# Kernel tuning notes

Measured on AMD Instinct MI355X. Metric: run time of the kernel, lower is better.

Reference implementation:

```python
import jax, jax.numpy as jnp
import numpy as np

B, S, D, A = 16, 4096, 2048, 2048

def setup_inputs() -> dict:
    key = jax.random.key(0)
    k1, k2, k3, k4 = jax.random.split(key, 4)
    encode_state = jax.random.normal(k1, (B, S, D), dtype=jnp.float32)
    hid_state = jax.random.normal(k2, (B, D), dtype=jnp.float32)
    W = jax.random.normal(k3, (A, D), dtype=jnp.float32) * (1.0 / np.sqrt(D))
    b = jax.random.normal(k4, (A,), dtype=jnp.float32) * 0.01
    return {"encode_state": encode_state, "hid_state": hid_state, "W": W, "b": b}

def reference(encode_state, hid_state, W, b):
    # project both encoder states and decoder hidden state: y = x @ W.T + b
    enc_proj = jnp.einsum('bsd,ad->bsa', encode_state, W) + b   # [B,S,A]
    hid_proj = jnp.einsum('bd,ad->ba', hid_state, W) + b        # [B,A]
    scores = jnp.einsum('bsa,ba->bs', enc_proj, hid_proj)       # [B,S]
    probs = jax.nn.softmax(scores, axis=1)                      # softmax over seq dim
    context_vector = jnp.einsum('bs,bsd->bd', probs, encode_state)  # [B,D]
    return (scores, context_vector)
```

## Files before the change

### kernel.cpp

```cpp
#include <hip/hip_runtime.h>
#include <cstddef>

#define BB 16
#define SS 4096
#define DD 2048
#define AA 2048
#define CH 128
#define ACH 64

__global__ __launch_bounds__(256) void hp_kernel(
    const float* __restrict__ hid, const float* __restrict__ W,
    const float* __restrict__ bias, float* __restrict__ hp) {
  int gw   = (blockIdx.x * 256 + threadIdx.x) >> 6;
  int lane = threadIdx.x & 63;
  int a = gw;
  const float4* Wr = reinterpret_cast<const float4*>(W + (size_t)a * DD);
  float acc[BB];
#pragma unroll
  for (int b = 0; b < BB; ++b) acc[b] = 0.f;
#pragma unroll
  for (int k = 0; k < 8; ++k) {
    float4 w4 = Wr[lane + 64 * k];
#pragma unroll
    for (int b = 0; b < BB; ++b) {
      float4 h4 = reinterpret_cast<const float4*>(hid + b * DD)[lane + 64 * k];
      acc[b] += w4.x * h4.x + w4.y * h4.y + w4.z * h4.z + w4.w * h4.w;
    }
  }
  float bi = bias[a];
#pragma unroll
  for (int b = 0; b < BB; ++b) {
    float s = acc[b];
#pragma unroll
    for (int off = 32; off; off >>= 1) s += __shfl_xor(s, off, 64);
    if (lane == 0) hp[b * AA + a] = s + bi;
  }
}

__global__ __launch_bounds__(256) void vpart_kernel(
    const float* __restrict__ hp, const float* __restrict__ W,
    float* __restrict__ vpart) {
  int t  = threadIdx.x;
  int ac = blockIdx.x & 63;
  int dc = blockIdx.x >> 6;
  int d0 = dc * 1024 + 4 * t;
  float4 acc[BB];
#pragma unroll
  for (int b = 0; b < BB; ++b) acc[b] = make_float4(0.f, 0.f, 0.f, 0.f);
  int abase = ac * 32;
  for (int i = 0; i < 32; ++i) {
    int a = abase + i;
    float4 w4 = *reinterpret_cast<const float4*>(W + (size_t)a * DD + d0);
#pragma unroll
    for (int b = 0; b < BB; ++b) {
      float h = hp[b * AA + a];
      acc[b].x += h * w4.x; acc[b].y += h * w4.y;
      acc[b].z += h * w4.z; acc[b].w += h * w4.w;
    }
  }
#pragma unroll
  for (int b = 0; b < BB; ++b)
    *reinterpret_cast<float4*>(vpart + (size_t)(ac * BB + b) * DD + d0) = acc[b];
}

__global__ __launch_bounds__(256) void c_kernel(
    const float* __restrict__ hp, const float* __restrict__ bias,
    float* __restrict__ cvec) {
  int b = blockIdx.x, t = threadIdx.x;
  float s = 0.f;
  for (int i = t; i < AA; i += 256) s += bias[i] * hp[b * AA + i];
#pragma unroll
  for (int off = 32; off; off >>= 1) s += __shfl_xor(s, off, 64);
  __shared__ float red[4];
  if ((t & 63) == 0) red[t >> 6] = s;
  __syncthreads();
  if (t == 0) cvec[b] = red[0] + red[1] + red[2] + red[3];
}

__global__ __launch_bounds__(256) void reducev_kernel(
    const float* __restrict__ vpart, float* __restrict__ v) {
  int i = blockIdx.x * 256 + threadIdx.x;
  float s = 0.f;
#pragma unroll
  for (int c = 0; c < ACH; ++c) s += vpart[(size_t)c * (BB * DD) + i];
  v[i] = s;
}

__global__ __launch_bounds__(256) void fused_kernel(
    const float* __restrict__ enc, const float* __restrict__ v,
    const float* __restrict__ cvec, float* __restrict__ scores,
    float* __restrict__ mpart, float* __restrict__ lpart,
    float* __restrict__ ctxpart) {
  int gw   = blockIdx.x * 4 + (threadIdx.x >> 6);
  int lane = threadIdx.x & 63;
  int b  = gw >> 7;
  int ch = gw & (CH - 1);
  const float4* vp = reinterpret_cast<const float4*>(v + b * DD);
  float4 vf[8];
#pragma unroll
  for (int k = 0; k < 8; ++k) vf[k] = vp[lane + 64 * k];
  float cb = cvec[b];
  float4 acc[8];
#pragma unroll
  for (int k = 0; k < 8; ++k) acc[k] = make_float4(0.f, 0.f, 0.f, 0.f);
  float m = -1e30f, l = 0.f, myscore = 0.f;
  size_t rowbase = (size_t)(b * SS + ch * 32) * DD;
  for (int r = 0; r < 32; ++r) {
    const float4* ep = reinterpret_cast<const float4*>(enc + rowbase + (size_t)r * DD);
    float4 e[8];
#pragma unroll
    for (int k = 0; k < 8; ++k) e[k] = ep[lane + 64 * k];
    float dot = 0.f;
#pragma unroll
    for (int k = 0; k < 8; ++k)
      dot += e[k].x * vf[k].x + e[k].y * vf[k].y + e[k].z * vf[k].z + e[k].w * vf[k].w;
#pragma unroll
    for (int off = 32; off; off >>= 1) dot += __shfl_xor(dot, off, 64);
    float score = dot + cb;
    if (lane == r) myscore = score;
    float mnew  = fmaxf(m, score);
    float scale = __expf(m - mnew);
    float p     = __expf(score - mnew);
    l = l * scale + p;
#pragma unroll
    for (int k = 0; k < 8; ++k) {
      acc[k].x = acc[k].x * scale + p * e[k].x;
      acc[k].y = acc[k].y * scale + p * e[k].y;
      acc[k].z = acc[k].z * scale + p * e[k].z;
      acc[k].w = acc[k].w * scale + p * e[k].w;
    }
    m = mnew;
  }
  if (lane < 32) scores[b * SS + ch * 32 + lane] = myscore;
  if (lane == 0) { mpart[gw] = m; lpart[gw] = l; }
  float4* cp = reinterpret_cast<float4*>(ctxpart + (size_t)gw * DD);
#pragma unroll
  for (int k = 0; k < 8; ++k) cp[lane + 64 * k] = acc[k];
}

__global__ __launch_bounds__(128) void mstats_kernel(
    const float* __restrict__ mpart, const float* __restrict__ lpart,
    float* __restrict__ wnorm) {
  int b = blockIdx.x, t = threadIdx.x;
  float mt = mpart[b * CH + t];
  float lt = lpart[b * CH + t];
  float M = mt;
#pragma unroll
  for (int off = 32; off; off >>= 1) M = fmaxf(M, __shfl_xor(M, off, 64));
  __shared__ float sm[2];
  if ((t & 63) == 0) sm[t >> 6] = M;
  __syncthreads();
  M = fmaxf(sm[0], sm[1]);
  float w  = __expf(mt - M);
  float lw = lt * w;
#pragma unroll
  for (int off = 32; off; off >>= 1) lw += __shfl_xor(lw, off, 64);
  __shared__ float sl[2];
  if ((t & 63) == 0) sl[t >> 6] = lw;
  __syncthreads();
  float L = sl[0] + sl[1];
  wnorm[b * CH + t] = w / L;
}

__global__ __launch_bounds__(256) void combine1_kernel(
    const float* __restrict__ ctxpart, const float* __restrict__ wnorm,
    float* __restrict__ part2) {
  int b = blockIdx.x >> 3;
  int g = blockIdx.x & 7;
  int t = threadIdx.x;
  float4 a0 = make_float4(0.f, 0.f, 0.f, 0.f);
  float4 a1 = make_float4(0.f, 0.f, 0.f, 0.f);
  for (int i = 0; i < 16; ++i) {
    int c = g * 16 + i;
    float w = wnorm[b * CH + c];
    const float4* cp = reinterpret_cast<const float4*>(ctxpart + (size_t)(b * CH + c) * DD);
    float4 e0 = cp[t];
    float4 e1 = cp[t + 256];
    a0.x += w * e0.x; a0.y += w * e0.y; a0.z += w * e0.z; a0.w += w * e0.w;
    a1.x += w * e1.x; a1.y += w * e1.y; a1.z += w * e1.z; a1.w += w * e1.w;
  }
  float4* o = reinterpret_cast<float4*>(part2 + (size_t)(b * 8 + g) * DD);
  o[t] = a0;
  o[t + 256] = a1;
}

__global__ __launch_bounds__(256) void combine2_kernel(
    const float* __restrict__ part2, float* __restrict__ ctx) {
  int i = blockIdx.x * 256 + threadIdx.x;
  int b = i >> 11;
  int d = i & 2047;
  float s = 0.f;
#pragma unroll
  for (int g = 0; g < 8; ++g) s += part2[(size_t)(b * 8 + g) * DD + d];
  ctx[i] = s;
}

extern "C" void kernel_launch(void* const* d_in, const int* in_sizes, int n_in,
                              void* d_out, int out_size, void* d_ws, size_t ws_size,
                              hipStream_t stream) {
  const float* enc  = (const float*)d_in[0];
  const float* hid  = (const float*)d_in[1];
  const float* W    = (const float*)d_in[2];
  const float* bias = (const float*)d_in[3];

  float* out_scores = (float*)d_out;
  float* out_ctx    = (float*)d_out + BB * SS;

  float* ws    = (float*)d_ws;
  float* hp    = ws;
  float* vpart = hp + BB * AA;
  float* v     = vpart + ACH * BB * DD;
  float* cvec  = v + BB * DD;
  float* mpart = cvec + BB;
  float* lpart = mpart + BB * CH;
  float* wnorm = lpart + BB * CH;
  float* ctxp  = wnorm + BB * CH;
  float* part2 = ctxp + (size_t)BB * CH * DD;

  hipLaunchKernelGGL(hp_kernel,      dim3(512), dim3(256), 0, stream, hid, W, bias, hp);
  hipLaunchKernelGGL(vpart_kernel,   dim3(128), dim3(256), 0, stream, hp, W, vpart);
  hipLaunchKernelGGL(c_kernel,       dim3(16),  dim3(256), 0, stream, hp, bias, cvec);
  hipLaunchKernelGGL(reducev_kernel, dim3(128), dim3(256), 0, stream, vpart, v);
  hipLaunchKernelGGL(fused_kernel,   dim3(512), dim3(256), 0, stream,
                     enc, v, cvec, out_scores, mpart, lpart, ctxp);
  hipLaunchKernelGGL(mstats_kernel,  dim3(16),  dim3(128), 0, stream, mpart, lpart, wnorm);
  hipLaunchKernelGGL(combine1_kernel, dim3(128), dim3(256), 0, stream, ctxp, wnorm, part2);
  hipLaunchKernelGGL(combine2_kernel, dim3(128), dim3(256), 0, stream, part2, out_ctx);
}
```

Before: 205.3 us.

## Double-buffer encoder rows, halve rows per wave, store partial contexts as bf16

The fused attention kernel now handles 16 rows per wave instead of 32, doubling the grid, and prefetches the next encoder row into a second register buffer while it computes on the current one. The v vector is reloaded from memory on each step instead of being kept in registers, and launch bounds ask for 4 blocks per CU to raise occupancy. Per-wave partial contexts are written as packed bf16, halving that intermediate traffic, and the combine and stats kernels are adjusted for 256 chunks. The cost is bf16 rounding in the context partials, plus twice as much partial data to reduce.

```diff
diff --git a/kernel.cpp b/kernel.cpp
--- a/kernel.cpp
+++ b/kernel.cpp
@@ -1,12 +1,19 @@
 #include <hip/hip_runtime.h>
+#include <hip/hip_bf16.h>
 #include <cstddef>
 
 #define BB 16
 #define SS 4096
 #define DD 2048
 #define AA 2048
-#define CH 128
+#define NR 16
+#define CH 256
 #define ACH 64
+
+__device__ inline unsigned int pk_bf16(float a, float b) {
+  __hip_bfloat162 h2 = __float22bfloat162_rn(make_float2(a, b));
+  return *reinterpret_cast<unsigned int*>(&h2);
+}
 
 __global__ __launch_bounds__(256) void hp_kernel(
     const float* __restrict__ hid, const float* __restrict__ W,
@@ -86,59 +93,78 @@
   v[i] = s;
 }
 
-__global__ __launch_bounds__(256) void fused_kernel(
+__global__ __launch_bounds__(256, 4) void fused_kernel(
     const float* __restrict__ enc, const float* __restrict__ v,
     const float* __restrict__ cvec, float* __restrict__ scores,
     float* __restrict__ mpart, float* __restrict__ lpart,
-    float* __restrict__ ctxpart) {
+    unsigned int* __restrict__ ctxpart ) {
   int gw   = blockIdx.x * 4 + (threadIdx.x >> 6);
   int lane = threadIdx.x & 63;
-  int b  = gw >> 7;
+  int b  = gw >> 8;
   int ch = gw & (CH - 1);
   const float4* vp = reinterpret_cast<const float4*>(v + b * DD);
-  float4 vf[8];
-#pragma unroll
-  for (int k = 0; k < 8; ++k) vf[k] = vp[lane + 64 * k];
   float cb = cvec[b];
   float4 acc[8];
 #pragma unroll
   for (int k = 0; k < 8; ++k) acc[k] = make_float4(0.f, 0.f, 0.f, 0.f);
   float m = -1e30f, l = 0.f, myscore = 0.f;
-  size_t rowbase = (size_t)(b * SS + ch * 32) * DD;
-  for (int r = 0; r < 32; ++r) {
-    const float4* ep = reinterpret_cast<const float4*>(enc + rowbase + (size_t)r * DD);
-    float4 e[8];
-#pragma unroll
-    for (int k = 0; k < 8; ++k) e[k] = ep[lane + 64 * k];
-    float dot = 0.f;
-#pragma unroll
-    for (int k = 0; k < 8; ++k)
-      dot += e[k].x * vf[k].x + e[k].y * vf[k].y + e[k].z * vf[k].z + e[k].w * vf[k].w;
-#pragma unroll
-    for (int off = 32; off; off >>= 1) dot += __shfl_xor(dot, off, 64);
-    float score = dot + cb;
-    if (lane == r) myscore = score;
-    float mnew  = fmaxf(m, score);
-    float scale = __expf(m - mnew);
-    float p     = __expf(score - mnew);
-    l = l * scale + p;
-#pragma unroll
-    for (int k = 0; k < 8; ++k) {
-      acc[k].x = acc[k].x * scale + p * e[k].x;
-      acc[k].y = acc[k].y * scale + p * e[k].y;
-      acc[k].z = acc[k].z * scale + p * e[k].z;
-      acc[k].w = acc[k].w * scale + p * e[k].w;
-    }
-    m = mnew;
-  }
-  if (lane < 32) scores[b * SS + ch * 32 + lane] = myscore;
+  const float4* rowp = reinterpret_cast<const float4*>(
+      enc + (size_t)(b * SS + ch * NR) * DD);
+  float4 eA[8], eB[8];
+#pragma unroll
+  for (int k = 0; k < 8; ++k) eA[k] = rowp[lane + 64 * k];
+
+#define STEP(CUR, NXT, R)                                                     \
+  {                                                                           \
+    int rn = ((R) + 1 < NR) ? (R) + 1 : (R);                                  \
+    _Pragma("unroll")                                                         \
+    for (int k = 0; k < 8; ++k)                                               \
+      NXT[k] = rowp[(size_t)rn * 512 + lane + 64 * k];                        \
+    float dot = 0.f;                                                          \
+    _Pragma("unroll")                                                         \
+    for (int k = 0; k < 8; ++k) {                                             \
+      float4 vv = vp[lane + 64 * k];                                          \
+      dot += CUR[k].x * vv.x + CUR[k].y * vv.y + CUR[k].z * vv.z +            \
+             CUR[k].w * vv.w;                                                 \
+    }                                                                         \
+    _Pragma("unroll")                                                         \
+    for (int off = 32; off; off >>= 1) dot += __shfl_xor(dot, off, 64);       \
+    float score = dot + cb;                                                   \
+    if (lane == (R)) myscore = score;                                         \
+    float mnew  = fmaxf(m, score);                                            \
+    float scale = __expf(m - mnew);                                           \
+    float p     = __expf(score - mnew);                                       \
+    l = l * scale + p;                                                        \
+    _Pragma("unroll")                                                         \
+    for (int k = 0; k < 8; ++k) {                                             \
+      acc[k].x = acc[k].x * scale + p * CUR[k].x;                             \
+      acc[k].y = acc[k].y * scale + p * CUR[k].y;                             \
+      acc[k].z = acc[k].z * scale + p * CUR[k].z;                             \
+      acc[k].w = acc[k].w * scale + p * CUR[k].w;                             \
+    }                                                                         \
+    m = mnew;                                                                 \
+  }
+
+#pragma unroll
+  for (int rr = 0; rr < NR; rr += 2) {
+    STEP(eA, eB, rr)
+    STEP(eB, eA, rr + 1)
+  }
+#undef STEP
+
+  if (lane < NR) scores[b * SS + ch * NR + lane] = myscore;
   if (lane == 0) { mpart[gw] = m; lpart[gw] = l; }
-  float4* cp = reinterpret_cast<float4*>(ctxpart + (size_t)gw * DD);
-#pragma unroll
-  for (int k = 0; k < 8; ++k) cp[lane + 64 * k] = acc[k];
-}
-
-__global__ __launch_bounds__(128) void mstats_kernel(
+  uint2* cp = reinterpret_cast<uint2*>(ctxpart) + (size_t)gw * 512;
+#pragma unroll
+  for (int k = 0; k < 8; ++k) {
+    uint2 u;
+    u.x = pk_bf16(acc[k].x, acc[k].y);
+    u.y = pk_bf16(acc[k].z, acc[k].w);
+    cp[lane + 64 * k] = u;
+  }
+}
+
+__global__ __launch_bounds__(256) void mstats_kernel(
     const float* __restrict__ mpart, const float* __restrict__ lpart,
     float* __restrict__ wnorm) {
   int b = blockIdx.x, t = threadIdx.x;
@@ -147,41 +173,47 @@
   float M = mt;
 #pragma unroll
   for (int off = 32; off; off >>= 1) M = fmaxf(M, __shfl_xor(M, off, 64));
-  __shared__ float sm[2];
+  __shared__ float sm[4];
   if ((t & 63) == 0) sm[t >> 6] = M;
   __syncthreads();
-  M = fmaxf(sm[0], sm[1]);
+  M = fmaxf(fmaxf(sm[0], sm[1]), fmaxf(sm[2], sm[3]));
   float w  = __expf(mt - M);
   float lw = lt * w;
 #pragma unroll
   for (int off = 32; off; off >>= 1) lw += __shfl_xor(lw, off, 64);
-  __shared__ float sl[2];
+  __shared__ float sl[4];
   if ((t & 63) == 0) sl[t >> 6] = lw;
   __syncthreads();
-  float L = sl[0] + sl[1];
+  float L = sl[0] + sl[1] + sl[2] + sl[3];
   wnorm[b * CH + t] = w / L;
 }
 
 __global__ __launch_bounds__(256) void combine1_kernel(
-    const float* __restrict__ ctxpart, const float* __restrict__ wnorm,
+    const unsigned int* __restrict__ ctxpart, const float* __restrict__ wnorm,
     float* __restrict__ part2) {
-  int b = blockIdx.x >> 3;
-  int g = blockIdx.x & 7;
+  int b = blockIdx.x >> 4;
+  int g = blockIdx.x & 15;
   int t = threadIdx.x;
-  float4 a0 = make_float4(0.f, 0.f, 0.f, 0.f);
-  float4 a1 = make_float4(0.f, 0.f, 0.f, 0.f);
+  float a0 = 0.f, a1 = 0.f, a2 = 0.f, a3 = 0.f;
+  float a4 = 0.f, a5 = 0.f, a6 = 0.f, a7 = 0.f;
   for (int i = 0; i < 16; ++i) {
     int c = g * 16 + i;
     float w = wnorm[b * CH + c];
-    const float4* cp = reinterpret_cast<const float4*>(ctxpart + (size_t)(b * CH + c) * DD);
-    float4 e0 = cp[t];
-    float4 e1 = cp[t + 256];
-    a0.x += w * e0.x; a0.y += w * e0.y; a0.z += w * e0.z; a0.w += w * e0.w;
-    a1.x += w * e1.x; a1.y += w * e1.y; a1.z += w * e1.z; a1.w += w * e1.w;
-  }
-  float4* o = reinterpret_cast<float4*>(part2 + (size_t)(b * 8 + g) * DD);
-  o[t] = a0;
-  o[t + 256] = a1;
+    const uint4* p = reinterpret_cast<const uint4*>(
+        ctxpart + (size_t)(b * CH + c) * (DD / 2));
+    uint4 q = p[t];
+    a0 += w * __uint_as_float(q.x << 16);
+    a1 += w * __uint_as_float(q.x & 0xffff0000u);
+    a2 += w * __uint_as_float(q.y << 16);
+    a3 += w * __uint_as_float(q.y & 0xffff0000u);
+    a4 += w * __uint_as_float(q.z << 16);
+    a5 += w * __uint_as_float(q.z & 0xffff0000u);
+    a6 += w * __uint_as_float(q.w << 16);
+    a7 += w * __uint_as_float(q.w & 0xffff0000u);
+  }
+  float4* o = reinterpret_cast<float4*>(part2 + (size_t)(b * 16 + g) * DD + 8 * t);
+  o[0] = make_float4(a0, a1, a2, a3);
+  o[1] = make_float4(a4, a5, a6, a7);
 }
 
 __global__ __launch_bounds__(256) void combine2_kernel(
@@ -191,7 +223,7 @@
   int d = i & 2047;
   float s = 0.f;
 #pragma unroll
-  for (int g = 0; g < 8; ++g) s += part2[(size_t)(b * 8 + g) * DD + d];
+  for (int g = 0; g < 16; ++g) s += part2[(size_t)(b * 16 + g) * DD + d];
   ctx[i] = s;
 }
 
@@ -214,16 +246,16 @@
   float* mpart = cvec + BB;
   float* lpart = mpart + BB * CH;
   float* wnorm = lpart + BB * CH;
-  float* ctxp  = wnorm + BB * CH;
-  float* part2 = ctxp + (size_t)BB * CH * DD;
-
-  hipLaunchKernelGGL(hp_kernel,      dim3(512), dim3(256), 0, stream, hid, W, bias, hp);
-  hipLaunchKernelGGL(vpart_kernel,   dim3(128), dim3(256), 0, stream, hp, W, vpart);
-  hipLaunchKernelGGL(c_kernel,       dim3(16),  dim3(256), 0, stream, hp, bias, cvec);
-  hipLaunchKernelGGL(reducev_kernel, dim3(128), dim3(256), 0, stream, vpart, v);
-  hipLaunchKernelGGL(fused_kernel,   dim3(512), dim3(256), 0, stream,
+  unsigned int* ctxp = (unsigned int*)(wnorm + BB * CH);
+  float* part2 = (float*)(ctxp + (size_t)BB * CH * DD / 2);
+
+  hipLaunchKernelGGL(hp_kernel,      dim3(512),  dim3(256), 0, stream, hid, W, bias, hp);
+  hipLaunchKernelGGL(vpart_kernel,   dim3(128),  dim3(256), 0, stream, hp, W, vpart);
+  hipLaunchKernelGGL(c_kernel,       dim3(16),   dim3(256), 0, stream, hp, bias, cvec);
+  hipLaunchKernelGGL(reducev_kernel, dim3(128),  dim3(256), 0, stream, vpart, v);
+  hipLaunchKernelGGL(fused_kernel,   dim3(1024), dim3(256), 0, stream,
                      enc, v, cvec, out_scores, mpart, lpart, ctxp);
-  hipLaunchKernelGGL(mstats_kernel,  dim3(16),  dim3(128), 0, stream, mpart, lpart, wnorm);
-  hipLaunchKernelGGL(combine1_kernel, dim3(128), dim3(256), 0, stream, ctxp, wnorm, part2);
+  hipLaunchKernelGGL(mstats_kernel,  dim3(16),   dim3(256), 0, stream, mpart, lpart, wnorm);
+  hipLaunchKernelGGL(combine1_kernel, dim3(256), dim3(256), 0, stream, ctxp, wnorm, part2);
   hipLaunchKernelGGL(combine2_kernel, dim3(128), dim3(256), 0, stream, part2, out_ctx);
 }
```

Measured after the change: 449.7 us. +119.0%, slower.

## Halve rows per wave, lazily rescale softmax, store bf16 partials, merge small kernels

Applied to the files above, without the earlier changes.

The fused streaming kernel now handles 16 rows per wave with double the waves, for more parallelism over the encoder read. Online softmax now rescales the accumulator only when the score exceeds the running max by more than 40, which drops most per-row exp and multiply work. Context partials are stored as packed bf16 to halve the partial write and read traffic. The small kernels are merged: c and reducev become one finalize launch, and mstats plus the two combine passes become one epilogue, cutting launches from eight to five. The cost is bf16 rounding in the partial context sums and more partial rows to reduce.

```diff
diff --git a/kernel.cpp b/kernel.cpp
--- a/kernel.cpp
+++ b/kernel.cpp
@@ -1,12 +1,19 @@
 #include <hip/hip_runtime.h>
+#include <hip/hip_bf16.h>
 #include <cstddef>
 
 #define BB 16
 #define SS 4096
 #define DD 2048
 #define AA 2048
-#define CH 128
+#define NR 16
+#define CH 256
 #define ACH 64
+
+__device__ inline unsigned int pk_bf16(float a, float b) {
+  __hip_bfloat162 h2 = __float22bfloat162_rn(make_float2(a, b));
+  return *reinterpret_cast<unsigned int*>(&h2);
+}
 
 __global__ __launch_bounds__(256) void hp_kernel(
     const float* __restrict__ hid, const float* __restrict__ W,
@@ -63,136 +70,131 @@
     *reinterpret_cast<float4*>(vpart + (size_t)(ac * BB + b) * DD + d0) = acc[b];
 }
 
-__global__ __launch_bounds__(256) void c_kernel(
-    const float* __restrict__ hp, const float* __restrict__ bias,
+__global__ __launch_bounds__(256) void finalize_kernel(
+    const float* __restrict__ vpart, const float* __restrict__ hp,
+    const float* __restrict__ bias, float* __restrict__ v,
     float* __restrict__ cvec) {
-  int b = blockIdx.x, t = threadIdx.x;
-  float s = 0.f;
-  for (int i = t; i < AA; i += 256) s += bias[i] * hp[b * AA + i];
-#pragma unroll
-  for (int off = 32; off; off >>= 1) s += __shfl_xor(s, off, 64);
-  __shared__ float red[4];
-  if ((t & 63) == 0) red[t >> 6] = s;
-  __syncthreads();
-  if (t == 0) cvec[b] = red[0] + red[1] + red[2] + red[3];
-}
-
-__global__ __launch_bounds__(256) void reducev_kernel(
-    const float* __restrict__ vpart, float* __restrict__ v) {
-  int i = blockIdx.x * 256 + threadIdx.x;
-  float s = 0.f;
-#pragma unroll
-  for (int c = 0; c < ACH; ++c) s += vpart[(size_t)c * (BB * DD) + i];
-  v[i] = s;
+  if (blockIdx.x < 128) {
+    int i = blockIdx.x * 256 + threadIdx.x;
+    float s = 0.f;
+#pragma unroll
+    for (int c = 0; c < ACH; ++c) s += vpart[(size_t)c * (BB * DD) + i];
+    v[i] = s;
+  } else {
+    int b = blockIdx.x - 128;
+    int t = threadIdx.x;
+    float s = 0.f;
+    for (int i = t; i < AA; i += 256) s += bias[i] * hp[b * AA + i];
+#pragma unroll
+    for (int off = 32; off; off >>= 1) s += __shfl_xor(s, off, 64);
+    __shared__ float red[4];
+    if ((t & 63) == 0) red[t >> 6] = s;
+    __syncthreads();
+    if (t == 0) cvec[b] = red[0] + red[1] + red[2] + red[3];
+  }
 }
 
 __global__ __launch_bounds__(256) void fused_kernel(
     const float* __restrict__ enc, const float* __restrict__ v,
     const float* __restrict__ cvec, float* __restrict__ scores,
     float* __restrict__ mpart, float* __restrict__ lpart,
-    float* __restrict__ ctxpart) {
+    unsigned int* __restrict__ ctxpart ) {
   int gw   = blockIdx.x * 4 + (threadIdx.x >> 6);
   int lane = threadIdx.x & 63;
-  int b  = gw >> 7;
+  int b  = gw >> 8;
   int ch = gw & (CH - 1);
-  const float4* vp = reinterpret_cast<const float4*>(v + b * DD);
-  float4 vf[8];
-#pragma unroll
-  for (int k = 0; k < 8; ++k) vf[k] = vp[lane + 64 * k];
+  const float4* vp = reinterpret_cast<const float4*>(v + (size_t)b * DD);
   float cb = cvec[b];
   float4 acc[8];
 #pragma unroll
   for (int k = 0; k < 8; ++k) acc[k] = make_float4(0.f, 0.f, 0.f, 0.f);
-  float m = -1e30f, l = 0.f, myscore = 0.f;
-  size_t rowbase = (size_t)(b * SS + ch * 32) * DD;
-  for (int r = 0; r < 32; ++r) {
-    const float4* ep = reinterpret_cast<const float4*>(enc + rowbase + (size_t)r * DD);
+  float m_s = -1e30f;
+  float l = 0.f, myscore = 0.f;
+  const float4* rowp = reinterpret_cast<const float4*>(
+      enc + (size_t)(b * SS + ch * NR) * DD);
+
+#pragma unroll
+  for (int r = 0; r < NR; ++r) {
     float4 e[8];
 #pragma unroll
-    for (int k = 0; k < 8; ++k) e[k] = ep[lane + 64 * k];
+    for (int k = 0; k < 8; ++k) e[k] = rowp[(size_t)r * 512 + lane + 64 * k];
     float dot = 0.f;
 #pragma unroll
-    for (int k = 0; k < 8; ++k)
-      dot += e[k].x * vf[k].x + e[k].y * vf[k].y + e[k].z * vf[k].z + e[k].w * vf[k].w;
+    for (int k = 0; k < 8; ++k) {
+      float4 vv = vp[lane + 64 * k];
+      dot += e[k].x * vv.x + e[k].y * vv.y + e[k].z * vv.z + e[k].w * vv.w;
+    }
 #pragma unroll
     for (int off = 32; off; off >>= 1) dot += __shfl_xor(dot, off, 64);
     float score = dot + cb;
     if (lane == r) myscore = score;
-    float mnew  = fmaxf(m, score);
-    float scale = __expf(m - mnew);
-    float p     = __expf(score - mnew);
-    l = l * scale + p;
+    if (score > m_s + 40.f) {
+      float rs = __expf(m_s - score);
+      l *= rs;
+#pragma unroll
+      for (int k = 0; k < 8; ++k) {
+        acc[k].x *= rs; acc[k].y *= rs; acc[k].z *= rs; acc[k].w *= rs;
+      }
+      m_s = score;
+    }
+    float p = __expf(score - m_s);
+    l += p;
 #pragma unroll
     for (int k = 0; k < 8; ++k) {
-      acc[k].x = acc[k].x * scale + p * e[k].x;
-      acc[k].y = acc[k].y * scale + p * e[k].y;
-      acc[k].z = acc[k].z * scale + p * e[k].z;
-      acc[k].w = acc[k].w * scale + p * e[k].w;
-    }
-    m = mnew;
-  }
-  if (lane < 32) scores[b * SS + ch * 32 + lane] = myscore;
-  if (lane == 0) { mpart[gw] = m; lpart[gw] = l; }
-  float4* cp = reinterpret_cast<float4*>(ctxpart + (size_t)gw * DD);
-#pragma unroll
-  for (int k = 0; k < 8; ++k) cp[lane + 64 * k] = acc[k];
-}
-
-__global__ __launch_bounds__(128) void mstats_kernel(
+      acc[k].x += p * e[k].x;
+      acc[k].y += p * e[k].y;
+      acc[k].z += p * e[k].z;
+      acc[k].w += p * e[k].w;
+    }
+  }
+
+  if (lane < NR) scores[b * SS + ch * NR + lane] = myscore;
+  if (lane == 0) { mpart[gw] = m_s; lpart[gw] = l; }
+  uint2* cp = reinterpret_cast<uint2*>(ctxpart) + (size_t)gw * 512;
+#pragma unroll
+  for (int k = 0; k < 8; ++k) {
+    uint2 u;
+    u.x = pk_bf16(acc[k].x, acc[k].y);
+    u.y = pk_bf16(acc[k].z, acc[k].w);
+    cp[lane + 64 * k] = u;
+  }
+}
+
+__global__ __launch_bounds__(256) void epilogue_kernel(
     const float* __restrict__ mpart, const float* __restrict__ lpart,
-    float* __restrict__ wnorm) {
-  int b = blockIdx.x, t = threadIdx.x;
+    const unsigned int* __restrict__ ctxpart, float* __restrict__ ctx) {
+  int b  = blockIdx.x >> 3;
+  int ds = blockIdx.x & 7;
+  int t  = threadIdx.x;
+  __shared__ float wsm[CH];
+  __shared__ float redm[4], redl[4];
   float mt = mpart[b * CH + t];
   float lt = lpart[b * CH + t];
   float M = mt;
 #pragma unroll
   for (int off = 32; off; off >>= 1) M = fmaxf(M, __shfl_xor(M, off, 64));
-  __shared__ float sm[2];
-  if ((t & 63) == 0) sm[t >> 6] = M;
+  if ((t & 63) == 0) redm[t >> 6] = M;
   __syncthreads();
-  M = fmaxf(sm[0], sm[1]);
+  M = fmaxf(fmaxf(redm[0], redm[1]), fmaxf(redm[2], redm[3]));
   float w  = __expf(mt - M);
   float lw = lt * w;
 #pragma unroll
   for (int off = 32; off; off >>= 1) lw += __shfl_xor(lw, off, 64);
-  __shared__ float sl[2];
-  if ((t & 63) == 0) sl[t >> 6] = lw;
+  if ((t & 63) == 0) redl[t >> 6] = lw;
   __syncthreads();
-  float L = sl[0] + sl[1];
-  wnorm[b * CH + t] = w / L;
-}
-
-__global__ __launch_bounds__(256) void combine1_kernel(
-    const float* __restrict__ ctxpart, const float* __restrict__ wnorm,
-    float* __restrict__ part2) {
-  int b = blockIdx.x >> 3;
-  int g = blockIdx.x & 7;
-  int t = threadIdx.x;
-  float4 a0 = make_float4(0.f, 0.f, 0.f, 0.f);
-  float4 a1 = make_float4(0.f, 0.f, 0.f, 0.f);
-  for (int i = 0; i < 16; ++i) {
-    int c = g * 16 + i;
-    float w = wnorm[b * CH + c];
-    const float4* cp = reinterpret_cast<const float4*>(ctxpart + (size_t)(b * CH + c) * DD);
-    float4 e0 = cp[t];
-    float4 e1 = cp[t + 256];
-    a0.x += w * e0.x; a0.y += w * e0.y; a0.z += w * e0.z; a0.w += w * e0.w;
-    a1.x += w * e1.x; a1.y += w * e1.y; a1.z += w * e1.z; a1.w += w * e1.w;
-  }
-  float4* o = reinterpret_cast<float4*>(part2 + (size_t)(b * 8 + g) * DD);
-  o[t] = a0;
-  o[t + 256] = a1;
-}
-
-__global__ __launch_bounds__(256) void combine2_kernel(
-    const float* __restrict__ part2, float* __restrict__ ctx) {
-  int i = blockIdx.x * 256 + threadIdx.x;
-  int b = i >> 11;
-  int d = i & 2047;
-  float s = 0.f;
-#pragma unroll
-  for (int g = 0; g < 8; ++g) s += part2[(size_t)(b * 8 + g) * DD + d];
-  ctx[i] = s;
+  float L = redl[0] + redl[1] + redl[2] + redl[3];
+  wsm[t] = w / L;
+  __syncthreads();
+  int du = ds * 128 + (t >> 1);
+  bool hi = (t & 1);
+  float acc = 0.f;
+  const unsigned int* base = ctxpart + (size_t)(b * CH) * (DD / 2) + du;
+  for (int c = 0; c < CH; ++c) {
+    unsigned int u = base[(size_t)c * (DD / 2)];
+    float e = __uint_as_float(hi ? (u & 0xffff0000u) : (u << 16));
+    acc += wsm[c] * e;
+  }
+  ctx[b * DD + ds * 256 + t] = acc;
 }
 
 extern "C" void kernel_launch(void* const* d_in, const int* in_sizes, int n_in,
@@ -213,17 +215,13 @@
   float* cvec  = v + BB * DD;
   float* mpart = cvec + BB;
   float* lpart = mpart + BB * CH;
-  float* wnorm = lpart + BB * CH;
-  float* ctxp  = wnorm + BB * CH;
-  float* part2 = ctxp + (size_t)BB * CH * DD;
-
-  hipLaunchKernelGGL(hp_kernel,      dim3(512), dim3(256), 0, stream, hid, W, bias, hp);
-  hipLaunchKernelGGL(vpart_kernel,   dim3(128), dim3(256), 0, stream, hp, W, vpart);
-  hipLaunchKernelGGL(c_kernel,       dim3(16),  dim3(256), 0, stream, hp, bias, cvec);
-  hipLaunchKernelGGL(reducev_kernel, dim3(128), dim3(256), 0, stream, vpart, v);
-  hipLaunchKernelGGL(fused_kernel,   dim3(512), dim3(256), 0, stream,
+  unsigned int* ctxp = (unsigned int*)(lpart + BB * CH);
+
+  hipLaunchKernelGGL(hp_kernel,       dim3(512),  dim3(256), 0, stream, hid, W, bias, hp);
+  hipLaunchKernelGGL(vpart_kernel,    dim3(128),  dim3(256), 0, stream, hp, W, vpart);
+  hipLaunchKernelGGL(finalize_kernel, dim3(144),  dim3(256), 0, stream, vpart, hp, bias, v, cvec);
+  hipLaunchKernelGGL(fused_kernel,    dim3(1024), dim3(256), 0, stream,
                      enc, v, cvec, out_scores, mpart, lpart, ctxp);
-  hipLaunchKernelGGL(mstats_kernel,  dim3(16),  dim3(128), 0, stream, mpart, lpart, wnorm);
-  hipLaunchKernelGGL(combine1_kernel, dim3(128), dim3(256), 0, stream, ctxp, wnorm, part2);
-  hipLaunchKernelGGL(combine2_kernel, dim3(128), dim3(256), 0, stream, part2, out_ctx);
-}
+  hipLaunchKernelGGL(epilogue_kernel, dim3(128),  dim3(256), 0, stream,
+                     mpart, lpart, ctxp, out_ctx);
+}
```

New measurement: 198.5 us. 3.3% less time.
